# Optimization experiments

Measured on AMD Instinct MI355X. Metric: run time of the kernel, lower is better.

The kernel has to match this reference:

```python
import jax, jax.numpy as jnp
import numpy as np

B, S, C = 2, 4096, 640
HEADS = 10
DH = C // HEADS  # 64
SCALE = 1.0 / np.sqrt(DH).astype(np.float32)


def setup_inputs() -> dict:
    key = jax.random.key(0)
    ks = jax.random.split(key, 5)
    w_std = 0.02
    return {
        "hidden_states": jax.random.normal(ks[0], (B, S, C), dtype=jnp.float32),
        "Wq": jax.random.normal(ks[1], (C, C), dtype=jnp.float32) * w_std,
        "Wk": jax.random.normal(ks[2], (C, C), dtype=jnp.float32) * w_std,
        "Wv": jax.random.normal(ks[3], (C, C), dtype=jnp.float32) * w_std,
        "Wo": jax.random.normal(ks[4], (C, C), dtype=jnp.float32) * w_std,
        "b_out": jnp.zeros((C,), dtype=jnp.float32),
    }


def _split_heads(x):
    # [B, S, C] -> [B, H, S, Dh]
    b, s, c = x.shape
    return x.reshape(b, s, HEADS, DH).transpose(0, 2, 1, 3)


def reference(hidden_states, Wq, Wk, Wv, Wo, b_out):
    residual = hidden_states
    # Linear projections (torch nn.Linear: x @ W.T), to_q/k/v have no bias
    q = jnp.einsum("bsc,dc->bsd", hidden_states, Wq)
    k = jnp.einsum("bsc,dc->bsd", hidden_states, Wk)
    v = jnp.einsum("bsc,dc->bsd", hidden_states, Wv)
    q = _split_heads(q)  # [B, H, S, Dh]
    k = _split_heads(k)
    v = _split_heads(v)
    # get_attention_scores: scaled QK^T + softmax (full O(S^2) matrix)
    scores = jnp.einsum("bhqd,bhkd->bhqk", q, k) * SCALE
    probs = jax.nn.softmax(scores, axis=-1)
    out = jnp.einsum("bhqk,bhkd->bhqd", probs, v)  # [B, H, S, Dh]
    # batch_to_head_dim: [B, H, S, Dh] -> [B, S, C]
    out = out.transpose(0, 2, 1, 3).reshape(hidden_states.shape)
    # to_out[0] Linear (with bias), to_out[1] Dropout = identity at eval
    out = jnp.einsum("bsc,dc->bsd", out, Wo) + b_out
    # residual_connection=True, rescale_output_factor=1.0
    return out + residual
```

## Files before the change

### kernel.cpp

```cpp
#include <hip/hip_runtime.h>
#include <stdint.h>
#include <stddef.h>

#define Bsz 2
#define Ssz 4096
#define Csz 640
#define Hn 10
#define Dh 64
#define NSPLIT 4
#define QROWS 81920
#define NITEMS 2560
#define PBLOCKS 1024

typedef __attribute__((ext_vector_type(8))) short bf16x8;
typedef __attribute__((ext_vector_type(4))) float f32x4;
typedef __attribute__((ext_vector_type(16))) float f32x16;
typedef __attribute__((ext_vector_type(2))) unsigned int u32x2;
typedef __attribute__((ext_vector_type(2))) float f32x2;

typedef __attribute__((address_space(1))) void as1_void;
typedef __attribute__((address_space(3))) void as3_void;

__device__ __forceinline__ void async16(const void* g, void* l) {
  __builtin_amdgcn_global_load_lds((as1_void*)(g), (as3_void*)(l), 16, 0, 0);
}

__device__ __forceinline__ ushort f2bf(float f) {
  union { float f; uint32_t u; } v; v.f = f;
  return (ushort)((v.u + 0x7FFFu + ((v.u >> 16) & 1u)) >> 16);
}

__device__ __forceinline__ uint32_t pack_bf16(float lo, float hi) {
  return __builtin_amdgcn_perm(__float_as_uint(hi), __float_as_uint(lo), 0x07060302u);
}

__device__ __forceinline__ float bf_lo(uint32_t u) {
  return __uint_as_float(u << 16);
}
__device__ __forceinline__ float bf_hi(uint32_t u) {
  return __uint_as_float(u & 0xFFFF0000u);
}

__device__ __forceinline__ float fast_exp2(float x) {
#if __has_builtin(__builtin_amdgcn_exp2f)
  return __builtin_amdgcn_exp2f(x);
#else
  return __exp2f(x);
#endif
}

#define QSCALE 0.1803368801111204f

__global__ __launch_bounds__(256) void cvt_all(
    const float* __restrict__ hs, const float* __restrict__ Wq,
    const float* __restrict__ Wk, const float* __restrict__ Wv,
    const float* __restrict__ Wo, ushort* __restrict__ Xbf,
    ushort* __restrict__ Wqb, ushort* __restrict__ Wkb,
    ushort* __restrict__ Wvb, ushort* __restrict__ Wob)
{
  int gb = blockIdx.x;
  const float* in;
  ushort* out;
  int i;
  if (gb < 5120) {
    in = hs; out = Xbf;
    i = gb * 256 + threadIdx.x;
  } else {
    int wj = gb - 5120;
    int mat = wj / 400;
    int rb = wj - mat * 400;
    in  = (mat == 0) ? Wq  : (mat == 1) ? Wk  : (mat == 2) ? Wv  : Wo;
    out = (mat == 0) ? Wqb : (mat == 1) ? Wkb : (mat == 2) ? Wvb : Wob;
    i = rb * 256 + threadIdx.x;
  }
  const float4 v = ((const float4*)in)[i];
  ushort4 o;
  o.x = f2bf(v.x); o.y = f2bf(v.y); o.z = f2bf(v.z); o.w = f2bf(v.w);
  ((ushort4*)out)[i] = o;
}

template<int MODE>
__global__ __launch_bounds__(256) void gemm_k(
    const ushort* __restrict__ A, const ushort* __restrict__ W0,
    const ushort* __restrict__ W1, const ushort* __restrict__ W2,
    ushort* __restrict__ Qh, ushort* __restrict__ Kh, ushort* __restrict__ Vt,
    const float* __restrict__ bias, const float* __restrict__ residual,
    float* __restrict__ outf)
{
  __shared__ ushort As[128 * 64];
  __shared__ ushort Bs[128 * 64];
  const int t = threadIdx.x;
  const int lane = t & 63;
  const int w = t >> 6;
  const int quad = lane >> 4;
  const int l15 = lane & 15;
  const int m0 = blockIdx.x * 128;
  const int wub = t & ~63;

  int n0, mat;
  const ushort* W;
  if (MODE == 0) {
    mat = blockIdx.y / 5;
    n0 = (blockIdx.y % 5) * 128;
    W = (mat == 0) ? W0 : ((mat == 1) ? W1 : W2);
  } else {
    mat = 0;
    n0 = blockIdx.y * 128;
    W = W0;
  }
  const int qm = (w >> 1) * 64;
  const int qn = (w & 1) * 64;

  f32x4 acc[4][4];
  const f32x4 zero4 = {0.f, 0.f, 0.f, 0.f};
#pragma unroll
  for (int i = 0; i < 4; ++i)
#pragma unroll
    for (int j = 0; j < 4; ++j) acc[i][j] = zero4;

  for (int k0 = 0; k0 < Csz; k0 += 64) {
    __syncthreads();
#pragma unroll
    for (int s = 0; s < 4; ++s) {
      int L = s * 256 + t;
      int row = L >> 3, pc = L & 7;
      int c = pc ^ (row & 7);
      async16(A + (size_t)(m0 + row) * Csz + k0 + c * 8,
              (char*)As + (s * 256 + wub) * 16);
    }
#pragma unroll
    for (int s = 0; s < 4; ++s) {
      int L = s * 256 + t;
      int row = L >> 3, pc = L & 7;
      int c = pc ^ (row & 7);
      async16(W + (size_t)(n0 + row) * Csz + k0 + c * 8,
              (char*)Bs + (s * 256 + wub) * 16);
    }
    __syncthreads();
#pragma unroll
    for (int ks = 0; ks < 2; ++ks) {
      bf16x8 af[4], bfr[4];
#pragma unroll
      for (int i = 0; i < 4; ++i) {
        int row = qm + i * 16 + l15;
        int pc = (ks * 4 + quad) ^ (row & 7);
        af[i] = *(const bf16x8*)(As + row * 64 + pc * 8);
      }
#pragma unroll
      for (int j = 0; j < 4; ++j) {
        int row = qn + j * 16 + l15;
        int pc = (ks * 4 + quad) ^ (row & 7);
        bfr[j] = *(const bf16x8*)(Bs + row * 64 + pc * 8);
      }
#pragma unroll
      for (int i = 0; i < 4; ++i)
#pragma unroll
        for (int j = 0; j < 4; ++j)
          acc[i][j] = __builtin_amdgcn_mfma_f32_16x16x32_bf16(af[i], bfr[j], acc[i][j], 0, 0, 0);
    }
  }

  if (MODE == 0) {
    if (mat < 2) {
      ushort* __restrict__ dst = (mat == 0) ? Qh : Kh;
      const float sc = (mat == 0) ? QSCALE : 1.0f;
#pragma unroll
      for (int j = 0; j < 4; ++j) {
        int n = n0 + qn + j * 16 + l15;
        int h = n >> 6, dh = n & 63;
#pragma unroll
        for (int i = 0; i < 4; ++i) {
#pragma unroll
          for (int r = 0; r < 4; ++r) {
            int m = m0 + qm + i * 16 + quad * 4 + r;
            int b = m >> 12, sidx = m & 4095;
            dst[(((size_t)b * Hn + h) * Ssz + sidx) * Dh + dh] = f2bf(acc[i][j][r] * sc);
          }
        }
      }
    } else {
#pragma unroll
      for (int j = 0; j < 4; ++j) {
        int n = n0 + qn + j * 16 + l15;
        int h = n >> 6, dh = n & 63;
#pragma unroll
        for (int i = 0; i < 4; ++i) {
          int mb = m0 + qm + i * 16 + quad * 4;
          int b = mb >> 12, sidx = mb & 4095;
          ushort4 pk;
          pk.x = f2bf(acc[i][j][0]); pk.y = f2bf(acc[i][j][1]);
          pk.z = f2bf(acc[i][j][2]); pk.w = f2bf(acc[i][j][3]);
          *(ushort4*)(Vt + (((size_t)b * Hn + h) * Dh + dh) * Ssz + sidx) = pk;
        }
      }
    }
  } else {
#pragma unroll
    for (int j = 0; j < 4; ++j) {
      int n = n0 + qn + j * 16 + l15;
      float bs = bias[n];
#pragma unroll
      for (int i = 0; i < 4; ++i) {
#pragma unroll
        for (int r = 0; r < 4; ++r) {
          int m = m0 + qm + i * 16 + quad * 4 + r;
          size_t idx = (size_t)m * Csz + n;
          outf[idx] = acc[i][j][r] + bs + residual[idx];
        }
      }
    }
  }
}

__global__ __launch_bounds__(256, 4) void attn_k(
    const ushort* __restrict__ Qh, const ushort* __restrict__ Kh,
    const ushort* __restrict__ Vt, ushort* __restrict__ Opart,
    float* __restrict__ lpart)
{
  __shared__ ushort Ks[2][64 * 64];
  __shared__ ushort Vs[2][64 * 64];

  const int t = threadIdx.x;
  const int lane = t & 63;
  const int w = t >> 6;
  const int l31 = lane & 31;
  const int hi = lane >> 5;

  int ka[4];
#pragma unroll
  for (int ks = 0; ks < 4; ++ks)
    ka[ks] = l31 * 128 + (((ks * 2 + hi) ^ (l31 & 7)) << 4);

  const int row8 = lane >> 3;
  const int pcs = lane & 7;

  f32x16 z16;
#pragma unroll
  for (int i = 0; i < 16; ++i) z16[i] = 0.f;

  const char* Kbase = (const char*)&Ks[0][0];
  const char* Vbase = (const char*)&Vs[0][0];

  for (int item = blockIdx.x; item < NITEMS; item += PBLOCKS) {
    const int jj = item >> 3;
    const int x = jj & 31;
    const int team = (item & 7) + ((jj >> 5) << 3);
    const int bh = team % 20;
    const int z = team / 20;

    const size_t qk_off = (size_t)bh * Ssz * Dh;
    const size_t v_off = (size_t)bh * Dh * Ssz;
    const int qbase = x * 128 + w * 32;
    const int kvbase = z * (Ssz / NSPLIT);

    bf16x8 qf[4];
    {
      int q = qbase + l31;
#pragma unroll
      for (int ks = 0; ks < 4; ++ks)
        qf[ks] = *(const bf16x8*)(Qh + qk_off + (size_t)q * Dh + ks * 16 + hi * 8);
    }

    f32x16 Oa[2];
    Oa[0] = z16; Oa[1] = z16;
    f32x2 lp2 = {0.f, 0.f};

#define STAGE(bi, kv)                                                          \
  {                                                                            \
    _Pragma("unroll") for (int s = 0; s < 2; ++s) {                            \
      int i = w * 2 + s;                                                       \
      int row = i * 8 + row8;                                                  \
      int c = pcs ^ (row & 7);                                                 \
      async16(Kh + qk_off + (size_t)(kvbase + (kv) + row) * Dh + c * 8,        \
              (char*)&Ks[bi][0] + i * 1024);                                   \
    }                                                                          \
    _Pragma("unroll") for (int s = 0; s < 2; ++s) {                            \
      int i = w * 2 + s;                                                       \
      int row = i * 8 + row8;                                                  \
      int c = pcs ^ (row & 7);                                                 \
      async16(Vt + v_off + (size_t)row * Ssz + kvbase + (kv) + c * 8,          \
              (char*)&Vs[bi][0] + i * 1024);                                   \
    }                                                                          \
  }

    STAGE(0, 0);

#define ITER(IT, CB, CBO, DO_STAGE)                                            \
  {                                                                            \
    asm volatile("s_barrier" ::: "memory");                                    \
    if (DO_STAGE) {                                                            \
      STAGE((CB) ^ 1, ((IT) + 1) * 64);                                        \
      asm volatile("s_waitcnt vmcnt(4)" ::: "memory");                         \
    } else {                                                                   \
      asm volatile("s_waitcnt vmcnt(0)" ::: "memory");                         \
    }                                                                          \
    asm volatile("s_barrier" ::: "memory");                                    \
    _Pragma("unroll")                                                          \
    for (int tau = 0; tau < 2; ++tau) {                                        \
      f32x16 Sq;                                                               \
      _Pragma("unroll")                                                        \
      for (int ks = 0; ks < 4; ++ks) {                                         \
        bf16x8 kf = *(const bf16x8*)(Kbase + (CBO) + tau * 4096 + ka[ks]);     \
        Sq = __builtin_amdgcn_mfma_f32_32x32x16_bf16(                          \
            kf, qf[ks], ks == 0 ? z16 : Sq, 0, 0, 0);                          \
      }                                                                        \
      uint32_t pk[8];                                                          \
      _Pragma("unroll")                                                        \
      for (int a = 0; a < 8; ++a) {                                            \
        float p0 = fast_exp2(Sq[2 * a]);                                       \
        float p1 = fast_exp2(Sq[2 * a + 1]);                                   \
        f32x2 pp = {p0, p1};                                                   \
        lp2 += pp;                                                             \
        pk[a] = pack_bf16(p0, p1);                                             \
      }                                                                        \
      _Pragma("unroll")                                                        \
      for (int k2 = 0; k2 < 2; ++k2) {                                         \
        const int ks2 = tau * 2 + k2;                                          \
        const int bA = (2 * ks2) & 3;                                          \
        const int bB = (2 * ks2 + 1) & 3;                                      \
        u32x2 r0 = __builtin_amdgcn_permlane32_swap(pk[2 * bA],                \
                                                    pk[2 * bB], false, false); \
        u32x2 r1 = __builtin_amdgcn_permlane32_swap(pk[2 * bA + 1],            \
                                                    pk[2 * bB + 1], false, false); \
        union { uint32_t u[4]; bf16x8 v; } pu;                                 \
        pu.u[0] = r0.x; pu.u[1] = r1.x;                                        \
        pu.u[2] = r0.y; pu.u[3] = r1.y;                                        \
        bf16x8 pf = pu.v;                                                      \
        _Pragma("unroll")                                                      \
        for (int mt = 0; mt < 2; ++mt) {                                       \
          bf16x8 vfr = *(const bf16x8*)(Vbase + (CBO) + mt * 4096 + ka[ks2]);  \
          Oa[mt] = __builtin_amdgcn_mfma_f32_32x32x16_bf16(vfr, pf, Oa[mt],    \
                                                           0, 0, 0);           \
        }                                                                      \
      }                                                                        \
    }                                                                          \
  }

    const int NH = (Ssz / NSPLIT) / 128;
    for (int itp = 0; itp < NH; ++itp) {
      const int it0 = itp * 2;
      ITER(it0, 0, 0, 1);
      ITER(it0 + 1, 1, 8192, (itp + 1 < NH));
    }
#undef ITER
#undef STAGE

    const size_t prow_base = (size_t)z * QROWS + (size_t)bh * Ssz;
    float l_part = lp2.x + lp2.y;
    float l_tot = l_part + __shfl_xor(l_part, 32, 64);
    int q = qbase + l31;
    if (hi == 0) lpart[prow_base + q] = l_tot;
    ushort* dst = Opart + (prow_base + q) * 64;
#pragma unroll
    for (int mt = 0; mt < 2; ++mt) {
#pragma unroll
      for (int gg = 0; gg < 4; ++gg) {
        int dh0 = mt * 32 + 8 * gg + 4 * hi;
        uint2 val;
        val.x = pack_bf16(Oa[mt][4 * gg + 0], Oa[mt][4 * gg + 1]);
        val.y = pack_bf16(Oa[mt][4 * gg + 2], Oa[mt][4 * gg + 3]);
        *(uint2*)(dst + dh0) = val;
      }
    }
  }
}

__global__ __launch_bounds__(256) void combine_k(
    const ushort* __restrict__ Opart, const float* __restrict__ lpart,
    ushort* __restrict__ attnb)
{
  int gid = blockIdx.x * 256 + threadIdx.x;
  int row = gid >> 4;
  int dh0 = (gid & 15) * 4;
  int bh = row >> 12, q = row & 4095;
  int b = bh / Hn, h = bh % Hn;
  float a0 = 0.f, a1 = 0.f, a2 = 0.f, a3 = 0.f, lsum = 0.f;
#pragma unroll
  for (int sp = 0; sp < NSPLIT; ++sp) {
    uint2 v = *(const uint2*)(Opart + ((size_t)sp * QROWS + row) * 64 + dh0);
    a0 += bf_lo(v.x); a1 += bf_hi(v.x);
    a2 += bf_lo(v.y); a3 += bf_hi(v.y);
    lsum += lpart[(size_t)sp * QROWS + row];
  }
  float inv = 1.0f / lsum;
  uint2 o;
  o.x = pack_bf16(a0 * inv, a1 * inv);
  o.y = pack_bf16(a2 * inv, a3 * inv);
  *(uint2*)(attnb + ((size_t)b * Ssz + q) * Csz + h * Dh + dh0) = o;
}

extern "C" void kernel_launch(void* const* d_in, const int* in_sizes, int n_in,
                              void* d_out, int out_size, void* d_ws, size_t ws_size,
                              hipStream_t stream) {
  (void)in_sizes; (void)n_in; (void)out_size; (void)ws_size;
  const float* hs = (const float*)d_in[0];
  const float* Wq = (const float*)d_in[1];
  const float* Wk = (const float*)d_in[2];
  const float* Wv = (const float*)d_in[3];
  const float* Wo = (const float*)d_in[4];
  const float* bo = (const float*)d_in[5];
  float* out = (float*)d_out;

  char* ws = (char*)d_ws;
  ushort* Xbf = (ushort*)(ws);
  ushort* Wqb = (ushort*)(ws + 10485760);
  ushort* Wkb = (ushort*)(ws + 10485760 + 819200);
  ushort* Wvb = (ushort*)(ws + 10485760 + 2 * 819200);
  ushort* Wob = (ushort*)(ws + 10485760 + 3 * 819200);
  ushort* Qh  = (ushort*)(ws + 13762560);
  ushort* Kh  = (ushort*)(ws + 13762560 + 10485760);
  ushort* Vt  = (ushort*)(ws + 13762560 + 2 * 10485760);
  ushort* attnb = (ushort*)(ws + 13762560 + 3 * 10485760);
  ushort* Opart = (ushort*)(ws + 55705600);
  float*  lpart = (float*)(ws + 55705600 + 41943040);

  hipLaunchKernelGGL(cvt_all, dim3(6720), dim3(256), 0, stream,
                     hs, Wq, Wk, Wv, Wo, Xbf, Wqb, Wkb, Wvb, Wob);

  hipLaunchKernelGGL((gemm_k<0>), dim3(64, 15), dim3(256), 0, stream,
                     Xbf, Wqb, Wkb, Wvb, Qh, Kh, Vt, (const float*)nullptr,
                     (const float*)nullptr, (float*)nullptr);
  hipLaunchKernelGGL(attn_k, dim3(PBLOCKS), dim3(256), 0, stream,
                     Qh, Kh, Vt, Opart, lpart);
  hipLaunchKernelGGL(combine_k, dim3(QROWS / 16), dim3(256), 0, stream,
                     Opart, lpart, attnb);
  hipLaunchKernelGGL((gemm_k<1>), dim3(64, 5), dim3(256), 0, stream,
                     attnb, Wob, (const ushort*)nullptr, (const ushort*)nullptr,
                     (ushort*)nullptr, (ushort*)nullptr, (ushort*)nullptr,
                     bo, hs, out);
}
```

Baseline: 238.3 us.

## Stage QKV epilogue through LDS for coalesced 16-byte stores; halve attention KV split

```diff
diff --git a/kernel.cpp b/kernel.cpp
--- a/kernel.cpp
+++ b/kernel.cpp
@@ -7,9 +7,9 @@
 #define Csz 640
 #define Hn 10
 #define Dh 64
-#define NSPLIT 4
+#define NSPLIT 2
 #define QROWS 81920
-#define NITEMS 2560
+#define NITEMS 1280
 #define PBLOCKS 1024
 
 typedef __attribute__((ext_vector_type(8))) short bf16x8;
@@ -87,8 +87,9 @@
     const float* __restrict__ bias, const float* __restrict__ residual,
     float* __restrict__ outf)
 {
-  __shared__ ushort As[128 * 64];
-  __shared__ ushort Bs[128 * 64];
+  __shared__ ushort SH[128 * 64 * 2];
+  ushort* As = SH;
+  ushort* Bs = SH + 8192;
   const int t = threadIdx.x;
   const int lane = t & 63;
   const int w = t >> 6;
@@ -161,37 +162,58 @@
   }
 
   if (MODE == 0) {
+    __syncthreads();
+    ushort* Tw = SH + w * 4096;
+    const int b = m0 >> 12;
+    const int sbase = (m0 & 4095) + qm;
+    const int rl = lane >> 3;
+    const int ck = lane & 7;
+
     if (mat < 2) {
-      ushort* __restrict__ dst = (mat == 0) ? Qh : Kh;
       const float sc = (mat == 0) ? QSCALE : 1.0f;
 #pragma unroll
       for (int j = 0; j < 4; ++j) {
-        int n = n0 + qn + j * 16 + l15;
-        int h = n >> 6, dh = n & 63;
+        int nl = j * 16 + l15;
+        int cn = nl >> 3, on = nl & 7;
 #pragma unroll
         for (int i = 0; i < 4; ++i) {
 #pragma unroll
           for (int r = 0; r < 4; ++r) {
-            int m = m0 + qm + i * 16 + quad * 4 + r;
-            int b = m >> 12, sidx = m & 4095;
-            dst[(((size_t)b * Hn + h) * Ssz + sidx) * Dh + dh] = f2bf(acc[i][j][r] * sc);
+            int ml = i * 16 + quad * 4 + r;
+            Tw[ml * 64 + (((cn ^ (ml & 7)) << 3) | on)] = f2bf(acc[i][j][r] * sc);
           }
         }
       }
+      ushort* __restrict__ dstp = (mat == 0) ? Qh : Kh;
+      const int h = (n0 + qn) >> 6;
+      const size_t base = ((size_t)(b * Hn + h) * Ssz + sbase) * Dh;
+#pragma unroll
+      for (int p = 0; p < 8; ++p) {
+        int row = p * 8 + rl;
+        uint4 vdat = *(const uint4*)(Tw + row * 64 + ((ck ^ (row & 7)) << 3));
+        *(uint4*)(dstp + base + (size_t)row * Dh + ck * 8) = vdat;
+      }
     } else {
 #pragma unroll
       for (int j = 0; j < 4; ++j) {
-        int n = n0 + qn + j * 16 + l15;
-        int h = n >> 6, dh = n & 63;
+        int nl = j * 16 + l15;
 #pragma unroll
         for (int i = 0; i < 4; ++i) {
-          int mb = m0 + qm + i * 16 + quad * 4;
-          int b = mb >> 12, sidx = mb & 4095;
-          ushort4 pk;
-          pk.x = f2bf(acc[i][j][0]); pk.y = f2bf(acc[i][j][1]);
-          pk.z = f2bf(acc[i][j][2]); pk.w = f2bf(acc[i][j][3]);
-          *(ushort4*)(Vt + (((size_t)b * Hn + h) * Dh + dh) * Ssz + sidx) = pk;
+          int ml = i * 16 + quad * 4;
+          int cm = ml >> 3, om = ml & 7;
+          ushort4 pk4;
+          pk4.x = f2bf(acc[i][j][0]); pk4.y = f2bf(acc[i][j][1]);
+          pk4.z = f2bf(acc[i][j][2]); pk4.w = f2bf(acc[i][j][3]);
+          *(ushort4*)(Tw + nl * 64 + (((cm ^ (nl & 7)) << 3) | om)) = pk4;
         }
+      }
+      const int h = (n0 + qn) >> 6;
+      const size_t base = (size_t)(b * Hn + h) * Dh * Ssz + sbase;
+#pragma unroll
+      for (int p = 0; p < 8; ++p) {
+        int row = p * 8 + rl;
+        uint4 vdat = *(const uint4*)(Tw + row * 64 + ((ck ^ (row & 7)) << 3));
+        *(uint4*)(Vt + base + (size_t)row * Ssz + ck * 8) = vdat;
       }
     }
   } else {
```

New measurement: 230.8 us. 3.2% less time.
